# Performance work log

Measured on AMD Instinct MI355X. Metric: run time of the kernel, lower is better.

The kernel has to match this reference:

```python
import jax, jax.numpy as jnp
import numpy as np

B, T, F, H = 256, 128, 128, 512

def setup_inputs() -> dict:
    key = jax.random.key(0)
    ks = jax.random.split(key, 20)
    def xavier(k, shape):
        fan_in, fan_out = shape[1], shape[0]
        lim = np.sqrt(6.0 / (fan_in + fan_out)).astype(np.float32)
        return jax.random.uniform(k, shape, jnp.float32, -lim, lim)
    inp = {
        "x": jax.random.normal(ks[0], (B, T, F), jnp.float32),
        "m": (jax.random.uniform(ks[1], (B, T, F)) < 0.8).astype(jnp.float32),
        "d": jax.random.uniform(ks[2], (B, T, F), jnp.float32),
        "target_x": jax.random.normal(ks[3], (B, T, F), jnp.float32),
        "target_mask": (jax.random.uniform(ks[4], (B, T, F)) < 0.2).astype(jnp.float32),
        # TemporalDecay h: W [H,F], b [H]
        "td_h_W": xavier(ks[5], (H, F)), "td_h_b": jnp.zeros((H,), jnp.float32),
        # TemporalDecay x (diag): W [F,F], b [F]
        "td_x_W": xavier(ks[6], (F, F)), "td_x_b": jnp.zeros((F,), jnp.float32),
        # hist_reg Linear(H->F)
        "hist_W": xavier(ks[7], (F, H)), "hist_b": jnp.zeros((F,), jnp.float32),
        "feat_W": xavier(ks[8], (F, F)), "feat_b": jnp.zeros((F,), jnp.float32),
        # weight_combine Linear(2F->F)
        "wc_W": xavier(ks[9], (F, 2 * F)), "wc_b": jnp.zeros((F,), jnp.float32),
        # LSTMCell(2F -> H), PyTorch gate order i,f,g,o
        "W_ih": xavier(ks[10], (4 * H, 2 * F)), "W_hh": xavier(ks[11], (4 * H, H)),
        "b_ih": jnp.zeros((4 * H,), jnp.float32), "b_hh": jnp.zeros((4 * H,), jnp.float32),
    }
    return inp

def _rits_forward(x, m, d, target_x, target_mask,
                  td_h_W, td_h_b, td_x_W, td_x_b,
                  hist_W, hist_b, feat_W, feat_b, wc_W, wc_b,
                  W_ih, W_hh, b_ih, b_hh):
    Bx, Tx, Fx = x.shape
    Hx = td_h_W.shape[0]
    feat_mask = (1.0 - jnp.eye(Fx, dtype=x.dtype))
    feat_Wm_T = (feat_W * feat_mask).T              # [F,F]
    td_x_diag = jnp.diagonal(td_x_W)                # diag mask reduces matmul to elementwise

    def step(carry, inp):
        h, c, loss = carry
        x_t, m_t, d_t, tgt_t, ev_t = inp
        gamma_h = jnp.exp(-jax.nn.relu(d_t @ td_h_W.T + td_h_b))    # [B,H]
        gamma_x = jnp.exp(-jax.nn.relu(d_t * td_x_diag + td_x_b))   # [B,F]
        h = h * gamma_h
        x_hist = h @ hist_W.T + hist_b                              # [B,F]
        x_c = m_t * x_t + (1.0 - m_t) * x_hist
        z_h = x_c @ feat_Wm_T + feat_b
        alpha = jax.nn.sigmoid(jnp.concatenate([gamma_x, m_t], axis=1) @ wc_W.T + wc_b)
        c_h = alpha * z_h + (1.0 - alpha) * x_hist
        c_c = m_t * x_t + (1.0 - m_t) * c_h
        inputs = jnp.concatenate([c_c, m_t], axis=1)                # [B,2F]
        gates = inputs @ W_ih.T + b_ih + h @ W_hh.T + b_hh          # [B,4H]
        i_g, f_g, g_g, o_g = jnp.split(gates, 4, axis=1)
        c = jax.nn.sigmoid(f_g) * c + jax.nn.sigmoid(i_g) * jnp.tanh(g_g)
        h = jax.nn.sigmoid(o_g) * jnp.tanh(c)
        denom = ev_t.sum() + 1e-8
        loss = loss + (((x_hist - tgt_t) ** 2 * ev_t).sum()
                       + ((z_h - tgt_t) ** 2 * ev_t).sum()
                       + ((c_h - tgt_t) ** 2 * ev_t).sum()) / denom
        return (h, c, loss), c_c

    h0 = jnp.zeros((Bx, Hx), x.dtype)
    c0 = jnp.zeros((Bx, Hx), x.dtype)
    tm = lambda a: jnp.swapaxes(a, 0, 1)  # time-major [T,B,F]
    (_, _, loss), imps = jax.lax.scan(
        step, (h0, c0, jnp.float32(0.0)),
        (tm(x), tm(m), tm(d), tm(target_x), tm(target_mask)))
    imputations = jnp.swapaxes(imps, 0, 1)  # [B,T,F]
    return imputations, loss / max(Tx, 1)

def reference(x, m, d, target_x, target_mask,
              td_h_W, td_h_b, td_x_W, td_x_b,
              hist_W, hist_b, feat_W, feat_b, wc_W, wc_b,
              W_ih, W_hh, b_ih, b_hh):
    return _rits_forward(x, m, d, target_x, target_mask,
                         td_h_W, td_h_b, td_x_W, td_x_b,
                         hist_W, hist_b, feat_W, feat_b, wc_W, wc_b,
                         W_ih, W_hh, b_ih, b_hh)
```

## Files before the change

### kernel.cpp

```cpp
#include <hip/hip_runtime.h>

#define DEVINL __device__ __forceinline__

namespace {
constexpr int B = 256, T = 128, F = 128, H = 512;
constexpr int NBLK = 256;
constexpr int NTHR = 1024;

constexpr size_t OFF_NUM    = 0;
constexpr size_t OFF_DEN    = 128;
constexpr size_t OFF_WQCC   = 256;
constexpr size_t OFF_WQH    = OFF_WQCC + 64 * 2048;
constexpr size_t OFF_FSCC   = OFF_WQH + 128 * 2048;
constexpr size_t OFF_FSCHG  = OFF_FSCC + 2048;
constexpr size_t OFF_HISTQ  = OFF_FSCHG + 2048;
constexpr size_t OFF_FSCH   = OFF_HISTQ + 128 * 128;
constexpr size_t OFF_TD2    = OFF_FSCH + 128;
constexpr size_t OFF_FEAT2  = OFF_TD2 + 64 * 512;
constexpr size_t OFF_WC2    = OFF_FEAT2 + 64 * 128;
constexpr size_t OFF_BSUM   = OFF_WC2 + 128 * 128;
constexpr size_t OFF_FDIAG  = OFF_BSUM + 2048;
constexpr size_t WS_WORDS   = OFF_FDIAG + 128;

constexpr float ACT_S  = 15.875f;
constexpr float DEQ_CC = 1.f / (127.f * 15.875f);
constexpr float DEQ_H  = 1.f / (127.f * 127.f);
}

typedef _Float16 h2_t __attribute__((ext_vector_type(2)));

DEVINL h2_t as_h2(unsigned u) { union { unsigned u; h2_t h; } c; c.u = u; return c.h; }
DEVINL unsigned pack2(float a, float b) {
  union { h2_t h; unsigned u; } c;
  c.h = h2_t{(_Float16)a, (_Float16)b};
  return c.u;
}

#if defined(__has_builtin)
#if __has_builtin(__builtin_amdgcn_fdot2)
#define HAVE_FDOT2 1
#endif
#if __has_builtin(__builtin_amdgcn_sdot4)
#define HAVE_SDOT4 1
#endif
#endif
#ifdef HAVE_FDOT2
DEVINL float fdot2(h2_t a, h2_t b, float c) { return __builtin_amdgcn_fdot2(a, b, c, false); }
#else
DEVINL float fdot2(h2_t a, h2_t b, float c) {
  return fmaf((float)a.x, (float)b.x, fmaf((float)a.y, (float)b.y, c));
}
#endif
#ifdef HAVE_SDOT4
DEVINL int sdot4(int a, int b, int c) { return __builtin_amdgcn_sdot4(a, b, c, false); }
#else
DEVINL int sdot4(int a, int b, int c) {
  return c + ((a << 24) >> 24) * ((b << 24) >> 24)
           + ((a << 16) >> 24) * ((b << 16) >> 24)
           + ((a << 8) >> 24) * ((b << 8) >> 24)
           + (a >> 24) * (b >> 24);
}
#endif

DEVINL float fast_sig(float x)  { return 1.f / (1.f + __expf(-x)); }
DEVINL float fast_tanh(float x) { return 1.f - 2.f / (1.f + __expf(2.f * x)); }

DEVINL float wave_sum(float v) {
#pragma unroll
  for (int s = 32; s; s >>= 1) v += __shfl_down(v, s, 64);
  return v;
}
DEVINL float wave_max(float v) {
#pragma unroll
  for (int s = 32; s; s >>= 1) v = fmaxf(v, __shfl_down(v, s, 64));
  return v;
}

__global__ void prep_f16(const float* __restrict__ td_h_W, const float* __restrict__ feat_W,
                         const float* __restrict__ wc_W, const float* __restrict__ b_ih,
                         const float* __restrict__ b_hh,
                         unsigned* __restrict__ wsu, float* __restrict__ wsf) {
  int idx = blockIdx.x * blockDim.x + threadIdx.x;
  if (idx < 32768) {
    const int k2 = idx >> 9, j = idx & 511;
    wsu[OFF_TD2 + idx] = pack2(td_h_W[j * 128 + 2 * k2], td_h_W[j * 128 + 2 * k2 + 1]);
  } else if (idx < 40960) {
    const int i = idx - 32768, k2 = i >> 7, f = i & 127;
    wsu[OFF_FEAT2 + i] = pack2(feat_W[f * 128 + 2 * k2], feat_W[f * 128 + 2 * k2 + 1]);
  } else if (idx < 57344) {
    const int i = idx - 40960, k2 = i >> 7, f = i & 127;
    wsu[OFF_WC2 + i] = pack2(wc_W[f * 256 + 2 * k2], wc_W[f * 256 + 2 * k2 + 1]);
  } else if (idx < 59392) {
    const int i = idx - 57344, unit = i >> 2, g = i & 3;
    wsf[OFF_BSUM + i] = b_ih[g * 512 + unit] + b_hh[g * 512 + unit];
  } else if (idx < 59520) {
    const int f = idx - 59392;
    wsf[OFF_FDIAG + f] = (float)(_Float16)feat_W[f * 129];
  }
}

__global__ void prep_quant_wih(const float* __restrict__ Wih,
                               unsigned* __restrict__ wq, float* __restrict__ fscc) {
  const int col = blockIdx.x;
  const int unit = col >> 2, g = col & 3;
  const float* src = Wih + (size_t)(g * 512 + unit) * 256;
  const int t = threadIdx.x;
  const float4 v = ((const float4*)src)[t];
  float mx = fmaxf(fmaxf(fabsf(v.x), fabsf(v.y)), fmaxf(fabsf(v.z), fabsf(v.w)));
  mx = wave_max(mx);
  mx = __shfl(mx, 0, 64);
  const float s = (mx > 0.f) ? 127.f / mx : 0.f;
  const int q0 = __float2int_rn(v.x * s), q1 = __float2int_rn(v.y * s);
  const int q2 = __float2int_rn(v.z * s), q3 = __float2int_rn(v.w * s);
  wq[t * 2048 + col] =
      (q0 & 0xFF) | ((q1 & 0xFF) << 8) | ((q2 & 0xFF) << 16) | ((q3 & 0xFF) << 24);
  if (t == 0) fscc[col] = mx * DEQ_CC;
}

__global__ void prep_quant_whh(const float* __restrict__ Whh,
                               unsigned* __restrict__ wq, float* __restrict__ fschg) {
  const int col = blockIdx.x;
  const int unit = col >> 2, g = col & 3;
  const float* src = Whh + (size_t)(g * 512 + unit) * 512;
  const int t = threadIdx.x;
  const float4 v = ((const float4*)src)[t];
  float mx = fmaxf(fmaxf(fabsf(v.x), fabsf(v.y)), fmaxf(fabsf(v.z), fabsf(v.w)));
  mx = wave_max(mx);
  __shared__ float wm[2];
  if ((t & 63) == 0) wm[t >> 6] = mx;
  __syncthreads();
  const float maxv = fmaxf(wm[0], wm[1]);
  const float s = (maxv > 0.f) ? 127.f / maxv : 0.f;
  const int q0 = __float2int_rn(v.x * s), q1 = __float2int_rn(v.y * s);
  const int q2 = __float2int_rn(v.z * s), q3 = __float2int_rn(v.w * s);
  wq[t * 2048 + col] =
      (q0 & 0xFF) | ((q1 & 0xFF) << 8) | ((q2 & 0xFF) << 16) | ((q3 & 0xFF) << 24);
  if (t == 0) fschg[col] = maxv * DEQ_H;
}

__global__ void prep_quant_hist(const float* __restrict__ histW,
                                unsigned* __restrict__ histq, float* __restrict__ fsch) {
  const int f = blockIdx.x;
  const float* src = histW + (size_t)f * 512;
  const int t = threadIdx.x;
  const float4 v = ((const float4*)src)[t];
  float mx = fmaxf(fmaxf(fabsf(v.x), fabsf(v.y)), fmaxf(fabsf(v.z), fabsf(v.w)));
  mx = wave_max(mx);
  __shared__ float wm[2];
  if ((t & 63) == 0) wm[t >> 6] = mx;
  __syncthreads();
  const float maxv = fmaxf(wm[0], wm[1]);
  const float s = (maxv > 0.f) ? 127.f / maxv : 0.f;
  const int q0 = __float2int_rn(v.x * s), q1 = __float2int_rn(v.y * s);
  const int q2 = __float2int_rn(v.z * s), q3 = __float2int_rn(v.w * s);
  histq[t * 128 + f] =
      (q0 & 0xFF) | ((q1 & 0xFF) << 8) | ((q2 & 0xFF) << 16) | ((q3 & 0xFF) << 24);
  if (t == 0) fsch[f] = maxv * DEQ_H;
}

__global__ void __launch_bounds__(1024) rits_batch(
    const float* __restrict__ x, const float* __restrict__ m, const float* __restrict__ d,
    const float* __restrict__ tx, const float* __restrict__ tmask,
    const float* __restrict__ td_h_b, const float* __restrict__ td_x_W,
    const float* __restrict__ td_x_b, const float* __restrict__ hist_b,
    const float* __restrict__ feat_b, const float* __restrict__ wc_b,
    const unsigned* __restrict__ wsu, const float* __restrict__ wsf,
    float* __restrict__ num, float* __restrict__ den, float* __restrict__ out)
{
  const int tid = threadIdx.x;
  const int row = blockIdx.x;
  const int unit = tid & 511;
  const int kh = tid >> 9;

  __shared__ unsigned actq[64];
  __shared__ int hq[128];
  __shared__ unsigned d2[64];
  __shared__ unsigned xc2[64];
  __shared__ unsigned gxm2[128];
  __shared__ float xrow[128], mrow[128], drow[128], txrow[128], evrow[128];
  __shared__ int   partI[1024];
  __shared__ float partZ[1024], partA[1024];
  __shared__ int4  partHc[512], partHh[512];
  __shared__ float redA[2], redB[2];

  const float4 bs    = *(const float4*)(wsf + OFF_BSUM + 4 * unit);
  const float4 fscc4 = *(const float4*)(wsf + OFF_FSCC + 4 * unit);
  const float4 fsch4 = *(const float4*)(wsf + OFF_FSCHG + 4 * unit);
  const float tdb = td_h_b[unit];
  const int fc = tid & 127;
  const float hb = hist_b[fc], fb = feat_b[fc], wb = wc_b[fc];
  const float fd = wsf[OFF_FDIAG + fc];
  const float dxw = td_x_W[fc * 129], dxb = td_x_b[fc];
  const float fsch_f = wsf[OFF_FSCH + fc];

  float h0 = 0.f, c0 = 0.f;

  for (int t = 0; t < T; ++t) {
    const int base = (row * T + t) * F;
    float xh_r = 0.f, xc_r = 0.f;

    if (tid < 640) {
      const int a = tid >> 7, f = tid & 127;
      const float v = (a == 0 ? x[base + f] : a == 1 ? m[base + f] : a == 2 ? d[base + f]
                       : a == 3 ? tx[base + f] : tmask[base + f]);
      if      (a == 0) xrow[f]  = v;
      else if (a == 1) mrow[f]  = v;
      else if (a == 2) drow[f]  = v;
      else if (a == 3) txrow[f] = v;
      else             evrow[f] = v;
    } else if (tid < 704) {
      const int k2 = tid - 640;
      d2[k2] = pack2(d[base + 2 * k2], d[base + 2 * k2 + 1]);
    } else if (tid < 768) {
      const int q = tid - 704;
      gxm2[64 + q] = pack2(m[base + 2 * q], m[base + 2 * q + 1]);
    } else if (tid < 800) {
      const int w = tid - 768;
      const int b4 = base + 4 * w;
      const int q0 = __float2int_rn(m[b4] * ACT_S);
      const int q1 = __float2int_rn(m[b4 + 1] * ACT_S);
      const int q2 = __float2int_rn(m[b4 + 2] * ACT_S);
      const int q3 = __float2int_rn(m[b4 + 3] * ACT_S);
      actq[32 + w] =
          (q0 & 0xFF) | ((q1 & 0xFF) << 8) | ((q2 & 0xFF) << 16) | ((q3 & 0xFF) << 24);
    }
    __syncthreads();

    if (tid < 512) {
      float g0 = tdb;
#pragma unroll 8
      for (int k2 = 0; k2 < 64; ++k2)
        g0 = fdot2(as_h2(wsu[OFF_TD2 + (k2 << 9) + tid]), as_h2(d2[k2]), g0);
      h0 *= __expf(-fmaxf(g0, 0.f));
      int q = __float2int_rn(h0 * 127.f);
      const int a1 = __shfl_down(q, 1, 64), a2 = __shfl_down(q, 2, 64), a3 = __shfl_down(q, 3, 64);
      if ((tid & 3) == 0)
        hq[tid >> 2] =
            (q & 0xFF) | ((a1 & 0xFF) << 8) | ((a2 & 0xFF) << 16) | ((a3 & 0xFF) << 24);
    }
    __syncthreads();

    {
      const int kq = tid >> 7;
      int isum = 0;
#pragma unroll 8
      for (int k = 0; k < 16; ++k) {
        const int k4 = kq * 16 + k;
        isum = sdot4((int)wsu[OFF_HISTQ + (k4 << 7) + fc], hq[k4], isum);
      }
      partI[tid] = isum;
    }
    __syncthreads();

    if (tid < 128) {
      int isum = 0;
#pragma unroll
      for (int i = 0; i < 8; ++i) isum += partI[tid + 128 * i];
      xh_r = fmaf((float)isum, fsch_f, hb);
      const float gx = __expf(-fmaxf(fmaf(drow[tid], dxw, dxb), 0.f));
      const float mv = mrow[tid];
      xc_r = mv * xrow[tid] + (1.f - mv) * xh_r;
      const float xcs = __shfl_down(xc_r, 1, 64);
      const float gxs = __shfl_down(gx, 1, 64);
      if (!(tid & 1)) {
        xc2[tid >> 1]  = pack2(xc_r, xcs);
        gxm2[tid >> 1] = pack2(gx, gxs);
      }
    }
    __syncthreads();

    {
      const int kq = tid >> 7;
      float zs = 0.f;
#pragma unroll 8
      for (int k = 0; k < 8; ++k) {
        const int k2 = kq * 8 + k;
        zs = fdot2(as_h2(wsu[OFF_FEAT2 + (k2 << 7) + fc]), as_h2(xc2[k2]), zs);
      }
      partZ[tid] = zs;
      float as = 0.f;
#pragma unroll 8
      for (int k = 0; k < 16; ++k) {
        const int k2 = kq * 16 + k;
        as = fdot2(as_h2(wsu[OFF_WC2 + (k2 << 7) + fc]), as_h2(gxm2[k2]), as);
      }
      partA[tid] = as;
    }
    __syncthreads();

    if (tid < 128) {
      float z = fb, aa = wb;
#pragma unroll
      for (int i = 0; i < 8; ++i) { z += partZ[tid + 128 * i]; aa += partA[tid + 128 * i]; }
      z -= xc_r * fd;
      const float al = fast_sig(aa);
      const float ch = al * z + (1.f - al) * xh_r;
      const float mv = mrow[tid];
      const float cc = mv * xrow[tid] + (1.f - mv) * ch;
      out[base + tid] = cc;
      const float ev = evrow[tid], tg = txrow[tid];
      const float e1 = xh_r - tg, e2 = z - tg, e3 = ch - tg;
      const float s1 = wave_sum(ev * (e1 * e1 + e2 * e2 + e3 * e3));
      const float s2 = wave_sum(ev);
      if ((tid & 63) == 0) { redA[tid >> 6] = s1; redB[tid >> 6] = s2; }
      int qc = __float2int_rn(fminf(fmaxf(cc, -8.f), 8.f) * ACT_S);
      const int c1s = __shfl_down(qc, 1, 64), c2s = __shfl_down(qc, 2, 64), c3s = __shfl_down(qc, 3, 64);
      if (!(tid & 3))
        actq[tid >> 2] =
            (qc & 0xFF) | ((c1s & 0xFF) << 8) | ((c2s & 0xFF) << 16) | ((c3s & 0xFF) << 24);
    }
    __syncthreads();

    {
      if (tid == 1023) {
        atomicAdd(&num[t], redA[0] + redA[1]);
        atomicAdd(&den[t], redB[0] + redB[1]);
      }
      int ci = 0, cf = 0, cg = 0, co = 0;
      const unsigned* wq = wsu + OFF_WQCC + 4 * unit;
#pragma unroll 8
      for (int k = 0; k < 32; ++k) {
        const int k4 = kh * 32 + k;
        const uint4 w = *(const uint4*)(wq + (k4 << 11));
        const int a0 = (int)actq[k4];
        ci = sdot4((int)w.x, a0, ci); cf = sdot4((int)w.y, a0, cf);
        cg = sdot4((int)w.z, a0, cg); co = sdot4((int)w.w, a0, co);
      }
      int hi = 0, hf = 0, hg = 0, ho = 0;
      const unsigned* wh = wsu + OFF_WQH + 4 * unit;
#pragma unroll 8
      for (int k = 0; k < 64; ++k) {
        const int k4 = kh * 64 + k;
        const uint4 w = *(const uint4*)(wh + (k4 << 11));
        const int a0 = hq[k4];
        hi = sdot4((int)w.x, a0, hi); hf = sdot4((int)w.y, a0, hf);
        hg = sdot4((int)w.z, a0, hg); ho = sdot4((int)w.w, a0, ho);
      }
      if (tid >= 512) {
        partHc[unit] = int4{ci, cf, cg, co};
        partHh[unit] = int4{hi, hf, hg, ho};
      }
      __syncthreads();
      if (tid < 512) {
        const int4 pc = partHc[unit], ph = partHh[unit];
        const float ai = bs.x + fscc4.x * (float)(ci + pc.x) + fsch4.x * (float)(hi + ph.x);
        const float af = bs.y + fscc4.y * (float)(cf + pc.y) + fsch4.y * (float)(hf + ph.y);
        const float ag = bs.z + fscc4.z * (float)(cg + pc.z) + fsch4.z * (float)(hg + ph.z);
        const float ao = bs.w + fscc4.w * (float)(co + pc.w) + fsch4.w * (float)(ho + ph.w);
        const float ig = fast_sig(ai), fg = fast_sig(af);
        const float gg = fast_tanh(ag), og = fast_sig(ao);
        c0 = fg * c0 + ig * gg;
        h0 = og * fast_tanh(c0);
      }
    }
    __syncthreads();
  }
}

__global__ void finalize(const float* __restrict__ num, const float* __restrict__ den,
                         float* __restrict__ out) {
  __shared__ float red[2];
  const int t = threadIdx.x;
  float v = num[t] / (den[t] + 1e-8f);
  v = wave_sum(v);
  if ((t & 63) == 0) red[t >> 6] = v;
  __syncthreads();
  if (t == 0) out[(size_t)B * T * F] = (red[0] + red[1]) / (float)T;
}

extern "C" void kernel_launch(void* const* d_in, const int* in_sizes, int n_in,
                              void* d_out, int out_size, void* d_ws, size_t ws_size,
                              hipStream_t stream) {
  const float* x      = (const float*)d_in[0];
  const float* m      = (const float*)d_in[1];
  const float* d      = (const float*)d_in[2];
  const float* tx     = (const float*)d_in[3];
  const float* tmask  = (const float*)d_in[4];
  const float* td_h_W = (const float*)d_in[5];
  const float* td_h_b = (const float*)d_in[6];
  const float* td_x_W = (const float*)d_in[7];
  const float* td_x_b = (const float*)d_in[8];
  const float* hist_W = (const float*)d_in[9];
  const float* hist_b = (const float*)d_in[10];
  const float* feat_W = (const float*)d_in[11];
  const float* feat_b = (const float*)d_in[12];
  const float* wc_W   = (const float*)d_in[13];
  const float* wc_b   = (const float*)d_in[14];
  const float* W_ih   = (const float*)d_in[15];
  const float* W_hh   = (const float*)d_in[16];
  const float* b_ih   = (const float*)d_in[17];
  const float* b_hh   = (const float*)d_in[18];

  float*    wsf = (float*)d_ws;
  unsigned* wsu = (unsigned*)d_ws;
  float*    out = (float*)d_out;

  if (ws_size < WS_WORDS * 4) return;

  hipMemsetAsync(d_ws, 0, 256 * sizeof(float), stream);
  prep_f16<<<dim3((59520 + 255) / 256), dim3(256), 0, stream>>>(
      td_h_W, feat_W, wc_W, b_ih, b_hh, wsu, wsf);
  prep_quant_wih<<<dim3(2048), dim3(64), 0, stream>>>(
      W_ih, wsu + OFF_WQCC, wsf + OFF_FSCC);
  prep_quant_whh<<<dim3(2048), dim3(128), 0, stream>>>(
      W_hh, wsu + OFF_WQH, wsf + OFF_FSCHG);
  prep_quant_hist<<<dim3(128), dim3(128), 0, stream>>>(
      hist_W, wsu + OFF_HISTQ, wsf + OFF_FSCH);
  rits_batch<<<dim3(NBLK), dim3(NTHR), 0, stream>>>(
      x, m, d, tx, tmask, td_h_b, td_x_W, td_x_b, hist_b, feat_b, wc_b,
      wsu, wsf, wsf + OFF_NUM, wsf + OFF_DEN, out);
  finalize<<<dim3(1), dim3(128), 0, stream>>>(wsf + OFF_NUM, wsf + OFF_DEN, out);
}
```

Before: 2.433 ms.

## Split each batch row across two cooperating blocks with tagged global-memory exchange

Each batch row is now processed by a pair of 512-thread blocks. Each block owns half of the hidden units and half of the features, and the halves of the quantized hidden state, the complement input and the cell-candidate activations are exchanged each step through tagged 64-bit atomic slots in workspace memory. The aim is to halve the per-block weight streaming and the serial work in the recurrent loop while using twice as many blocks. The exchange relies on both blocks of a pair being resident at the same time. A spin cap sets a dead flag and silently produces wrong values if the partner is not scheduled. The gamma_x computation also moves into the load phase.

After: 3.784 ms. +55.5%, slower.

```diff
diff --git a/kernel.cpp b/kernel.cpp
--- a/kernel.cpp
+++ b/kernel.cpp
@@ -4,8 +4,8 @@
 
 namespace {
 constexpr int B = 256, T = 128, F = 128, H = 512;
-constexpr int NBLK = 256;
-constexpr int NTHR = 1024;
+constexpr int NBLK = 512;
+constexpr int NTHR = 512;
 
 constexpr size_t OFF_NUM    = 0;
 constexpr size_t OFF_DEN    = 128;
@@ -20,11 +20,15 @@
 constexpr size_t OFF_WC2    = OFF_FEAT2 + 64 * 128;
 constexpr size_t OFF_BSUM   = OFF_WC2 + 128 * 128;
 constexpr size_t OFF_FDIAG  = OFF_BSUM + 2048;
-constexpr size_t WS_WORDS   = OFF_FDIAG + 128;
+constexpr size_t OFF_HXW    = OFF_FDIAG + 128;
+constexpr size_t OFF_XCW    = OFF_HXW + 256 * 128 * 2;
+constexpr size_t OFF_CCW    = OFF_XCW + 256 * 64 * 2;
+constexpr size_t WS_WORDS   = OFF_CCW + 256 * 32 * 2;
 
 constexpr float ACT_S  = 15.875f;
 constexpr float DEQ_CC = 1.f / (127.f * 15.875f);
 constexpr float DEQ_H  = 1.f / (127.f * 127.f);
+constexpr unsigned SPIN_CAP = 1u << 17;
 }
 
 typedef _Float16 h2_t __attribute__((ext_vector_type(2)));
@@ -74,6 +78,20 @@
 #pragma unroll
   for (int s = 32; s; s >>= 1) v = fmaxf(v, __shfl_down(v, s, 64));
   return v;
+}
+
+DEVINL void ex_store(unsigned long long* p, unsigned tag, unsigned val) {
+  __hip_atomic_store(p, ((unsigned long long)tag << 32) | (unsigned long long)val,
+                     __ATOMIC_RELAXED, __HIP_MEMORY_SCOPE_AGENT);
+}
+DEVINL unsigned ex_load(unsigned long long* p, unsigned tag, int* dead) {
+  if (*dead) return 0u;
+  unsigned long long v = 0; unsigned n = 0;
+  for (;;) {
+    v = __hip_atomic_load(p, __ATOMIC_RELAXED, __HIP_MEMORY_SCOPE_AGENT);
+    if ((unsigned)(v >> 32) == tag) return (unsigned)v;
+    if (++n > SPIN_CAP) { *dead = 1; return (unsigned)v; }
+  }
 }
 
 __global__ void prep_f16(const float* __restrict__ td_h_W, const float* __restrict__ feat_W,
@@ -158,7 +176,7 @@
   if (t == 0) fsch[f] = maxv * DEQ_H;
 }
 
-__global__ void __launch_bounds__(1024) rits_batch(
+__global__ void __launch_bounds__(512, 4) rits_batch(
     const float* __restrict__ x, const float* __restrict__ m, const float* __restrict__ d,
     const float* __restrict__ tx, const float* __restrict__ tmask,
     const float* __restrict__ td_h_b, const float* __restrict__ td_x_W,
@@ -168,80 +186,100 @@
     float* __restrict__ num, float* __restrict__ den, float* __restrict__ out)
 {
   const int tid = threadIdx.x;
-  const int row = blockIdx.x;
-  const int unit = tid & 511;
-  const int kh = tid >> 9;
+  const int row = blockIdx.x >> 1;
+  const int p   = blockIdx.x & 1;
+  const int pw  = 1 - p;
+  const int ob  = p * 256;
+  const int ofb = p * 64;
+  const int ul  = tid & 255;
+
+  unsigned long long* HXW = (unsigned long long*)(wsf + OFF_HXW) + (size_t)row * 128;
+  unsigned long long* XCW = (unsigned long long*)(wsf + OFF_XCW) + (size_t)row * 64;
+  unsigned long long* CCW = (unsigned long long*)(wsf + OFF_CCW) + (size_t)row * 32;
 
   __shared__ unsigned actq[64];
   __shared__ int hq[128];
   __shared__ unsigned d2[64];
   __shared__ unsigned xc2[64];
   __shared__ unsigned gxm2[128];
-  __shared__ float xrow[128], mrow[128], drow[128], txrow[128], evrow[128];
-  __shared__ int   partI[1024];
-  __shared__ float partZ[1024], partA[1024];
-  __shared__ int4  partHc[512], partHh[512];
-  __shared__ float redA[2], redB[2];
-
-  const float4 bs    = *(const float4*)(wsf + OFF_BSUM + 4 * unit);
-  const float4 fscc4 = *(const float4*)(wsf + OFF_FSCC + 4 * unit);
-  const float4 fsch4 = *(const float4*)(wsf + OFF_FSCHG + 4 * unit);
-  const float tdb = td_h_b[unit];
-  const int fc = tid & 127;
+  __shared__ float xrow[128], mrow[128], drow[128], txrow[128], evrow[128], gx_ls[128];
+  __shared__ int   partI[512];
+  __shared__ float partZ[512], partA[512];
+  __shared__ int4  partH[256];
+  __shared__ int dead;
+
+  const float4 bs    = *(const float4*)(wsf + OFF_BSUM + 4 * (ob + ul));
+  const float4 fscc4 = *(const float4*)(wsf + OFF_FSCC + 4 * (ob + ul));
+  const float4 fsch4 = *(const float4*)(wsf + OFF_FSCHG + 4 * (ob + ul));
+  const float tdb = td_h_b[ob + ul];
+  const int fc = ofb + (tid & 63);
   const float hb = hist_b[fc], fb = feat_b[fc], wb = wc_b[fc];
   const float fd = wsf[OFF_FDIAG + fc];
-  const float dxw = td_x_W[fc * 129], dxb = td_x_b[fc];
   const float fsch_f = wsf[OFF_FSCH + fc];
 
   float h0 = 0.f, c0 = 0.f;
+  if (tid == 0) dead = 0;
 
   for (int t = 0; t < T; ++t) {
+    const unsigned tag = (unsigned)(t + 1);
     const int base = (row * T + t) * F;
     float xh_r = 0.f, xc_r = 0.f;
 
-    if (tid < 640) {
-      const int a = tid >> 7, f = tid & 127;
-      const float v = (a == 0 ? x[base + f] : a == 1 ? m[base + f] : a == 2 ? d[base + f]
-                       : a == 3 ? tx[base + f] : tmask[base + f]);
-      if      (a == 0) xrow[f]  = v;
-      else if (a == 1) mrow[f]  = v;
-      else if (a == 2) drow[f]  = v;
-      else if (a == 3) txrow[f] = v;
-      else             evrow[f] = v;
-    } else if (tid < 704) {
-      const int k2 = tid - 640;
-      d2[k2] = pack2(d[base + 2 * k2], d[base + 2 * k2 + 1]);
-    } else if (tid < 768) {
-      const int q = tid - 704;
-      gxm2[64 + q] = pack2(m[base + 2 * q], m[base + 2 * q + 1]);
-    } else if (tid < 800) {
-      const int w = tid - 768;
-      const int b4 = base + 4 * w;
-      const int q0 = __float2int_rn(m[b4] * ACT_S);
-      const int q1 = __float2int_rn(m[b4 + 1] * ACT_S);
-      const int q2 = __float2int_rn(m[b4 + 2] * ACT_S);
-      const int q3 = __float2int_rn(m[b4 + 3] * ACT_S);
-      actq[32 + w] =
-          (q0 & 0xFF) | ((q1 & 0xFF) << 8) | ((q2 & 0xFF) << 16) | ((q3 & 0xFF) << 24);
-    }
-    __syncthreads();
-
-    if (tid < 512) {
+    for (int i = tid; i < 928; i += 512) {
+      if (i < 640) {
+        const int a = i >> 7, f = i & 127;
+        const float v = (a == 0 ? x[base + f] : a == 1 ? m[base + f] : a == 2 ? d[base + f]
+                         : a == 3 ? tx[base + f] : tmask[base + f]);
+        if      (a == 0) xrow[f]  = v;
+        else if (a == 1) mrow[f]  = v;
+        else if (a == 2) drow[f]  = v;
+        else if (a == 3) txrow[f] = v;
+        else             evrow[f] = v;
+      } else if (i < 704) {
+        const int k2 = i - 640;
+        d2[k2] = pack2(d[base + 2 * k2], d[base + 2 * k2 + 1]);
+      } else if (i < 768) {
+        const int q = i - 704;
+        gxm2[64 + q] = pack2(m[base + 2 * q], m[base + 2 * q + 1]);
+      } else if (i < 800) {
+        const int w = i - 768;
+        const int b4 = base + 4 * w;
+        const int q0 = __float2int_rn(m[b4] * ACT_S);
+        const int q1 = __float2int_rn(m[b4 + 1] * ACT_S);
+        const int q2 = __float2int_rn(m[b4 + 2] * ACT_S);
+        const int q3 = __float2int_rn(m[b4 + 3] * ACT_S);
+        actq[32 + w] =
+            (q0 & 0xFF) | ((q1 & 0xFF) << 8) | ((q2 & 0xFF) << 16) | ((q3 & 0xFF) << 24);
+      } else {
+        const int f = i - 800;
+        gx_ls[f] = __expf(-fmaxf(fmaf(d[base + f], td_x_W[f * 129], td_x_b[f]), 0.f));
+      }
+    }
+    __syncthreads();
+
+    if (tid < 256) {
       float g0 = tdb;
 #pragma unroll 8
       for (int k2 = 0; k2 < 64; ++k2)
-        g0 = fdot2(as_h2(wsu[OFF_TD2 + (k2 << 9) + tid]), as_h2(d2[k2]), g0);
+        g0 = fdot2(as_h2(wsu[OFF_TD2 + (k2 << 9) + ob + tid]), as_h2(d2[k2]), g0);
       h0 *= __expf(-fmaxf(g0, 0.f));
       int q = __float2int_rn(h0 * 127.f);
       const int a1 = __shfl_down(q, 1, 64), a2 = __shfl_down(q, 2, 64), a3 = __shfl_down(q, 3, 64);
-      if ((tid & 3) == 0)
-        hq[tid >> 2] =
+      if ((tid & 3) == 0) {
+        const int wd = p * 64 + (tid >> 2);
+        const unsigned wv =
             (q & 0xFF) | ((a1 & 0xFF) << 8) | ((a2 & 0xFF) << 16) | ((a3 & 0xFF) << 24);
+        hq[wd] = (int)wv;
+        ex_store(HXW + wd, tag, wv);
+      }
+    } else if (tid < 320) {
+      const int wd = pw * 64 + (tid - 256);
+      hq[wd] = (int)ex_load(HXW + wd, tag, &dead);
     }
     __syncthreads();
 
     {
-      const int kq = tid >> 7;
+      const int kq = tid >> 6;
       int isum = 0;
 #pragma unroll 8
       for (int k = 0; k < 16; ++k) {
@@ -252,25 +290,31 @@
     }
     __syncthreads();
 
-    if (tid < 128) {
+    if (tid < 64) {
       int isum = 0;
 #pragma unroll
-      for (int i = 0; i < 8; ++i) isum += partI[tid + 128 * i];
+      for (int i = 0; i < 8; ++i) isum += partI[tid + 64 * i];
       xh_r = fmaf((float)isum, fsch_f, hb);
-      const float gx = __expf(-fmaxf(fmaf(drow[tid], dxw, dxb), 0.f));
-      const float mv = mrow[tid];
-      xc_r = mv * xrow[tid] + (1.f - mv) * xh_r;
+      const float mv = mrow[fc];
+      xc_r = mv * xrow[fc] + (1.f - mv) * xh_r;
       const float xcs = __shfl_down(xc_r, 1, 64);
-      const float gxs = __shfl_down(gx, 1, 64);
       if (!(tid & 1)) {
-        xc2[tid >> 1]  = pack2(xc_r, xcs);
-        gxm2[tid >> 1] = pack2(gx, gxs);
-      }
+        const int idx = p * 32 + (tid >> 1);
+        const unsigned wv = pack2(xc_r, xcs);
+        xc2[idx] = wv;
+        ex_store(XCW + idx, tag, wv);
+      }
+    } else if (tid < 96) {
+      const int idx = pw * 32 + (tid - 64);
+      xc2[idx] = ex_load(XCW + idx, tag, &dead);
+    } else if (tid >= 128 && tid < 192) {
+      const int q = tid - 128;
+      gxm2[q] = pack2(gx_ls[2 * q], gx_ls[2 * q + 1]);
     }
     __syncthreads();
 
     {
-      const int kq = tid >> 7;
+      const int kq = tid >> 6;
       float zs = 0.f;
 #pragma unroll 8
       for (int k = 0; k < 8; ++k) {
@@ -288,65 +332,74 @@
     }
     __syncthreads();
 
-    if (tid < 128) {
+    if (tid < 64) {
       float z = fb, aa = wb;
 #pragma unroll
-      for (int i = 0; i < 8; ++i) { z += partZ[tid + 128 * i]; aa += partA[tid + 128 * i]; }
+      for (int i = 0; i < 8; ++i) { z += partZ[tid + 64 * i]; aa += partA[tid + 64 * i]; }
       z -= xc_r * fd;
       const float al = fast_sig(aa);
       const float ch = al * z + (1.f - al) * xh_r;
-      const float mv = mrow[tid];
-      const float cc = mv * xrow[tid] + (1.f - mv) * ch;
-      out[base + tid] = cc;
-      const float ev = evrow[tid], tg = txrow[tid];
+      const float mv = mrow[fc];
+      const float cc = mv * xrow[fc] + (1.f - mv) * ch;
+      out[base + fc] = cc;
+      const float ev = evrow[fc], tg = txrow[fc];
       const float e1 = xh_r - tg, e2 = z - tg, e3 = ch - tg;
       const float s1 = wave_sum(ev * (e1 * e1 + e2 * e2 + e3 * e3));
       const float s2 = wave_sum(ev);
-      if ((tid & 63) == 0) { redA[tid >> 6] = s1; redB[tid >> 6] = s2; }
+      if (tid == 0) { atomicAdd(&num[t], s1); atomicAdd(&den[t], s2); }
       int qc = __float2int_rn(fminf(fmaxf(cc, -8.f), 8.f) * ACT_S);
       const int c1s = __shfl_down(qc, 1, 64), c2s = __shfl_down(qc, 2, 64), c3s = __shfl_down(qc, 3, 64);
-      if (!(tid & 3))
-        actq[tid >> 2] =
+      if (!(tid & 3)) {
+        const int idx = p * 16 + (tid >> 2);
+        const unsigned wv =
             (qc & 0xFF) | ((c1s & 0xFF) << 8) | ((c2s & 0xFF) << 16) | ((c3s & 0xFF) << 24);
+        actq[idx] = wv;
+        ex_store(CCW + idx, tag, wv);
+      }
+    } else if (tid < 80) {
+      const int idx = pw * 16 + (tid - 64);
+      actq[idx] = ex_load(CCW + idx, tag, &dead);
     }
     __syncthreads();
 
     {
-      if (tid == 1023) {
-        atomicAdd(&num[t], redA[0] + redA[1]);
-        atomicAdd(&den[t], redB[0] + redB[1]);
-      }
+      const int kh = tid >> 8;
+      const unsigned* wq = wsu + OFF_WQCC + 4 * (ob + ul);
+      const unsigned* wh = wsu + OFF_WQH  + 4 * (ob + ul);
       int ci = 0, cf = 0, cg = 0, co = 0;
-      const unsigned* wq = wsu + OFF_WQCC + 4 * unit;
-#pragma unroll 8
-      for (int k = 0; k < 32; ++k) {
-        const int k4 = kh * 32 + k;
-        const uint4 w = *(const uint4*)(wq + (k4 << 11));
-        const int a0 = (int)actq[k4];
-        ci = sdot4((int)w.x, a0, ci); cf = sdot4((int)w.y, a0, cf);
-        cg = sdot4((int)w.z, a0, cg); co = sdot4((int)w.w, a0, co);
-      }
       int hi = 0, hf = 0, hg = 0, ho = 0;
-      const unsigned* wh = wsu + OFF_WQH + 4 * unit;
-#pragma unroll 8
-      for (int k = 0; k < 64; ++k) {
-        const int k4 = kh * 64 + k;
-        const uint4 w = *(const uint4*)(wh + (k4 << 11));
-        const int a0 = hq[k4];
-        hi = sdot4((int)w.x, a0, hi); hf = sdot4((int)w.y, a0, hf);
-        hg = sdot4((int)w.z, a0, hg); ho = sdot4((int)w.w, a0, ho);
-      }
-      if (tid >= 512) {
-        partHc[unit] = int4{ci, cf, cg, co};
-        partHh[unit] = int4{hi, hf, hg, ho};
+      if (kh == 0) {
+#pragma unroll 8
+        for (int w = 0; w < 64; ++w) {
+          const uint4 W = *(const uint4*)(wq + (w << 11));
+          const int a0 = (int)actq[w];
+          ci = sdot4((int)W.x, a0, ci); cf = sdot4((int)W.y, a0, cf);
+          cg = sdot4((int)W.z, a0, cg); co = sdot4((int)W.w, a0, co);
+        }
+#pragma unroll 8
+        for (int k = 0; k < 32; ++k) {
+          const uint4 W = *(const uint4*)(wh + (k << 11));
+          const int a0 = hq[k];
+          hi = sdot4((int)W.x, a0, hi); hf = sdot4((int)W.y, a0, hf);
+          hg = sdot4((int)W.z, a0, hg); ho = sdot4((int)W.w, a0, ho);
+        }
+      } else {
+#pragma unroll 8
+        for (int k = 32; k < 128; ++k) {
+          const uint4 W = *(const uint4*)(wh + (k << 11));
+          const int a0 = hq[k];
+          hi = sdot4((int)W.x, a0, hi); hf = sdot4((int)W.y, a0, hf);
+          hg = sdot4((int)W.z, a0, hg); ho = sdot4((int)W.w, a0, ho);
+        }
+        partH[ul] = int4{hi, hf, hg, ho};
       }
       __syncthreads();
-      if (tid < 512) {
-        const int4 pc = partHc[unit], ph = partHh[unit];
-        const float ai = bs.x + fscc4.x * (float)(ci + pc.x) + fsch4.x * (float)(hi + ph.x);
-        const float af = bs.y + fscc4.y * (float)(cf + pc.y) + fsch4.y * (float)(hf + ph.y);
-        const float ag = bs.z + fscc4.z * (float)(cg + pc.z) + fsch4.z * (float)(hg + ph.z);
-        const float ao = bs.w + fscc4.w * (float)(co + pc.w) + fsch4.w * (float)(ho + ph.w);
+      if (tid < 256) {
+        const int4 ph = partH[ul];
+        const float ai = bs.x + fscc4.x * (float)ci + fsch4.x * (float)(hi + ph.x);
+        const float af = bs.y + fscc4.y * (float)cf + fsch4.y * (float)(hf + ph.y);
+        const float ag = bs.z + fscc4.z * (float)cg + fsch4.z * (float)(hg + ph.z);
+        const float ao = bs.w + fscc4.w * (float)co + fsch4.w * (float)(ho + ph.w);
         const float ig = fast_sig(ai), fg = fast_sig(af);
         const float gg = fast_tanh(ag), og = fast_sig(ao);
         c0 = fg * c0 + ig * gg;
@@ -398,6 +451,7 @@
   if (ws_size < WS_WORDS * 4) return;
 
   hipMemsetAsync(d_ws, 0, 256 * sizeof(float), stream);
+  hipMemsetAsync(wsf + OFF_HXW, 0, (WS_WORDS - OFF_HXW) * 4, stream);
   prep_f16<<<dim3((59520 + 255) / 256), dim3(256), 0, stream>>>(
       td_h_W, feat_W, wc_W, b_ih, b_hh, wsu, wsf);
   prep_quant_wih<<<dim3(2048), dim3(64), 0, stream>>>(
```
